# Performance work log

Hardware: AMD Instinct MI355X
Metric: run time of the kernel (lower is better)

The kernel has to match this reference:

```python
import jax, jax.numpy as jnp
import numpy as np
from jax import lax

EPS = 1e-6


def _gaussian_blur(heatmaps, kernel_size):
    # heatmaps: (B, K, H, W). 2D Gaussian conv with 'same' padding, as in the torch code.
    if kernel_size % 2 == 0:
        kernel_size += 1
    B, K, H, W = heatmaps.shape
    sigma = (kernel_size - 1) / 6.0
    coords = jnp.arange(kernel_size, dtype=heatmaps.dtype) - (kernel_size - 1) / 2.0
    g = jnp.exp(-coords ** 2 / (2 * sigma ** 2))
    g = g / g.sum()
    kernel = (g[None, :] * g[:, None])[None, None]  # (1,1,ks,ks)
    pad = kernel_size // 2
    x = heatmaps.reshape(B * K, 1, H, W)
    out = lax.conv_general_dilated(
        x, kernel, window_strides=(1, 1), padding=[(pad, pad), (pad, pad)],
        dimension_numbers=('NCHW', 'OIHW', 'NCHW'))
    return out.reshape(B, K, H, W)


def _dark_forward(heatmaps, kernel_size):
    B, K, H, W = heatmaps.shape
    smooth = _gaussian_blur(heatmaps, kernel_size)
    flat = smooth.reshape(B, K, H * W)
    max_idx = jnp.argmax(flat, axis=-1)            # (B,K) int
    max_vals = jnp.max(flat, axis=-1)              # (B,K)
    y_int = max_idx // W
    x_int = max_idx % W

    # Gather 3x3 patches around the peak (clipped indices; invalid peaks masked below).
    off = jnp.arange(-1, 2)
    yy = jnp.clip(y_int[..., None, None] + off[:, None], 0, H - 1)   # (B,K,3,3)
    xx = jnp.clip(x_int[..., None, None] + off[None, :], 0, W - 1)   # (B,K,3,3)
    lin = (yy * W + xx).reshape(B, K, 9)
    p = jnp.take_along_axis(flat, lin, axis=-1).reshape(B, K, 3, 3)

    dx = (p[..., 1, 2] - p[..., 1, 0]) * 0.5
    dy = (p[..., 2, 1] - p[..., 0, 1]) * 0.5
    dxx = p[..., 1, 2] - 2.0 * p[..., 1, 1] + p[..., 1, 0]
    dyy = p[..., 2, 1] - 2.0 * p[..., 1, 1] + p[..., 0, 1]
    dxy = (p[..., 2, 2] - p[..., 2, 0] - p[..., 0, 2] + p[..., 0, 0]) * 0.25
    det = dxx * dyy - dxy * dxy

    boundary_ok = (x_int >= 1) & (x_int < W - 1) & (y_int >= 1) & (y_int < H - 1)
    valid = boundary_ok & (jnp.abs(det) >= EPS) & (dxx < 0)
    safe_det = jnp.where(valid, det, 1.0)
    off_x = jnp.where(valid, jnp.clip(-(dyy * dx - dxy * dy) / safe_det, -0.5, 0.5), 0.0)
    off_y = jnp.where(valid, jnp.clip(-(dxx * dy - dxy * dx) / safe_det, -0.5, 0.5), 0.0)

    x = jnp.clip(x_int.astype(heatmaps.dtype) + off_x, 0, W - 1)
    y = jnp.clip(y_int.astype(heatmaps.dtype) + off_y, 0, H - 1)
    coords = jnp.stack([x, y], axis=-1)            # (B,K,2)
    return coords, max_vals


def setup_inputs() -> dict:
    key = jax.random.key(0)
    heatmaps = jax.random.normal(key, (64, 17, 256, 192), dtype=jnp.float32)
    return {"heatmaps": heatmaps, "kernel_size": 11}


def reference(heatmaps, kernel_size):
    return _dark_forward(heatmaps, kernel_size)
```

## Files before the change

### kernel.cpp

```cpp
#include <hip/hip_runtime.h>
#include <math.h>

#define H 256
#define W 192
#define BK 1088
#define KS 11
#define NS 4
#define SR 64
#define RING 13

struct GaussW { float g[KS]; };

__device__ __forceinline__ float shflf(float v, int srcLane) {
  return __shfl(v, srcLane & 63, 64);
}

__global__ __launch_bounds__(256) void dark_fused(const float* __restrict__ hm,
                                                  float* __restrict__ out,
                                                  GaussW gw) {
  const int map  = blockIdx.x;
  const int wv   = threadIdx.x >> 6;
  const int lane = threadIdx.x & 63;
  const int y0   = wv * SR;
  const int rs   = y0 - 5;
  const int re   = y0 + SR + 4;
  const float* mbase = hm + (size_t)map * (H * W);
  const float* base  = mbase + 3 * lane;

  float ring[RING][3];

  if (rs >= 0) { const float* p = base + rs * W;
    ring[0][0] = p[0]; ring[0][1] = p[1]; ring[0][2] = p[2];
  } else { ring[0][0] = ring[0][1] = ring[0][2] = 0.f; }
  if (rs + 1 >= 0) { const float* p = base + (rs + 1) * W;
    ring[1][0] = p[0]; ring[1][1] = p[1]; ring[1][2] = p[2];
  } else { ring[1][0] = ring[1][1] = ring[1][2] = 0.f; }

  float bestv = -INFINITY;
  int   besti = 0x7fffffff;

  for (int rb = rs; rb <= re; rb += RING) {
    #pragma unroll
    for (int s = 0; s < RING; ++s) {
      const int rr = rb + s;
      if (rr <= re) {
        {
          const int nr = rr + 2;
          float* slot = ring[(s + 2) % RING];
          if (nr <= re && nr >= 0 && nr < H) {
            const float* p = base + nr * W;
            slot[0] = p[0]; slot[1] = p[1]; slot[2] = p[2];
          } else { slot[0] = slot[1] = slot[2] = 0.f; }
        }
        if (rr >= y0 + 5) {
          float v0 = 0.f, v1 = 0.f, v2 = 0.f;
          #pragma unroll
          for (int i = 0; i < KS; ++i) {
            const float* sl = ring[(s + 3 + i) % RING];
            const float gi = gw.g[i];
            v0 = fmaf(gi, sl[0], v0);
            v1 = fmaf(gi, sl[1], v1);
            v2 = fmaf(gi, sl[2], v2);
          }
          float w13[13];
          w13[5] = v0; w13[6] = v1; w13[7] = v2;
          const float m2b = shflf(v1, lane - 2), m2c = shflf(v2, lane - 2);
          const float m1a = shflf(v0, lane - 1), m1b = shflf(v1, lane - 1), m1c = shflf(v2, lane - 1);
          const float p1a = shflf(v0, lane + 1), p1b = shflf(v1, lane + 1), p1c = shflf(v2, lane + 1);
          const float p2a = shflf(v0, lane + 2), p2b = shflf(v1, lane + 2);
          const bool vm2 = (lane >= 2), vm1 = (lane >= 1);
          const bool vp1 = (lane <= 62), vp2 = (lane <= 61);
          w13[0]  = vm2 ? m2b : 0.f;  w13[1]  = vm2 ? m2c : 0.f;
          w13[2]  = vm1 ? m1a : 0.f;  w13[3]  = vm1 ? m1b : 0.f;  w13[4] = vm1 ? m1c : 0.f;
          w13[8]  = vp1 ? p1a : 0.f;  w13[9]  = vp1 ? p1b : 0.f;  w13[10] = vp1 ? p1c : 0.f;
          w13[11] = vp2 ? p2a : 0.f;  w13[12] = vp2 ? p2b : 0.f;
          const int y = rr - 5;
          #pragma unroll
          for (int c = 0; c < 3; ++c) {
            float hv = 0.f;
            #pragma unroll
            for (int j = 0; j < KS; ++j) hv = fmaf(gw.g[j], w13[c + j], hv);
            const int idx = y * W + 3 * lane + c;
            if (hv > bestv) { bestv = hv; besti = idx; }
          }
        }
      }
    }
  }

  #pragma unroll
  for (int off = 32; off; off >>= 1) {
    const float ov = __shfl_xor(bestv, off, 64);
    const int   oi = __shfl_xor(besti, off, 64);
    if (ov > bestv || (ov == bestv && oi < besti)) { bestv = ov; besti = oi; }
  }

  __shared__ float swv[NS];
  __shared__ int   swi[NS];
  __shared__ float hbuf[39];

  if (lane == 0) { swv[wv] = bestv; swi[wv] = besti; }
  __syncthreads();
  if (wv != 0) return;

  float bv = swv[0]; int bi = swi[0];
  #pragma unroll
  for (int k = 1; k < NS; ++k) {
    const float v = swv[k]; const int ix = swi[k];
    if (v > bv || (v == bv && ix < bi)) { bv = v; bi = ix; }
  }
  const int y = bi / W;
  const int x = bi - y * W;
  const bool interior = (x >= 1) && (x < W - 1) && (y >= 1) && (y < H - 1);

  if (interior) {
    if (lane < 39) {
      const int rl = lane / 3, dxc = lane % 3;
      const int rr = y - 6 + rl;
      const int cc = x - 1 + dxc;
      float hv = 0.f;
      if (rr >= 0 && rr < H) {
        const float* rowp = mbase + rr * W;
        #pragma unroll
        for (int k = 0; k < KS; ++k) {
          const int c2 = cc - 5 + k;
          const float vv = (c2 >= 0 && c2 < W) ? rowp[c2] : 0.f;
          hv = fmaf(gw.g[k], vv, hv);
        }
      }
      hbuf[lane] = hv;
    }
  }

  if (lane == 0) {
    float xf = (float)x, yf = (float)y;
    if (interior) {
      float p[3][3];
      for (int dy = 0; dy < 3; ++dy)
        for (int dx = 0; dx < 3; ++dx) {
          float acc = 0.f;
          #pragma unroll
          for (int i = 0; i < KS; ++i) acc = fmaf(gw.g[i], hbuf[(dy + i) * 3 + dx], acc);
          p[dy][dx] = acc;
        }
      const float d1x = (p[1][2] - p[1][0]) * 0.5f;
      const float d1y = (p[2][1] - p[0][1]) * 0.5f;
      const float dxx = p[1][2] - 2.f * p[1][1] + p[1][0];
      const float dyy = p[2][1] - 2.f * p[1][1] + p[0][1];
      const float dxy = (p[2][2] - p[2][0] - p[0][2] + p[0][0]) * 0.25f;
      const float det = dxx * dyy - dxy * dxy;
      if (fabsf(det) >= 1e-6f && dxx < 0.f) {
        float ox = -(dyy * d1x - dxy * d1y) / det;
        float oy = -(dxx * d1y - dxy * d1x) / det;
        ox = fminf(fmaxf(ox, -0.5f), 0.5f);
        oy = fminf(fmaxf(oy, -0.5f), 0.5f);
        xf += ox; yf += oy;
      }
    }
    xf = fminf(fmaxf(xf, 0.f), (float)(W - 1));
    yf = fminf(fmaxf(yf, 0.f), (float)(H - 1));
    out[2 * map]      = xf;
    out[2 * map + 1]  = yf;
    out[2 * BK + map] = bv;
  }
}

extern "C" void kernel_launch(void* const* d_in, const int* in_sizes, int n_in,
                              void* d_out, int out_size, void* d_ws, size_t ws_size,
                              hipStream_t stream) {
  const float* hm = (const float*)d_in[0];
  float* out = (float*)d_out;
  (void)d_ws; (void)ws_size;

  GaussW gw;
  {
    const double sig = (KS - 1) / 6.0;
    const float denom = (float)(2.0 * sig * sig);
    float g[KS]; float s = 0.f;
    for (int i = 0; i < KS; ++i) {
      const float c = (float)i - (float)((KS - 1) / 2);
      g[i] = expf(-(c * c) / denom);
      s += g[i];
    }
    for (int i = 0; i < KS; ++i) gw.g[i] = g[i] / s;
  }

  dark_fused<<<BK, 256, 0, stream>>>(hm, out, gw);
}
```

Baseline: 308.0 us.

## Scatter vertical blur into rolling accumulators with deeper row prefetch

Replaces the 13-row ring buffer, where each output row re-gathers 11 stored rows, with a scatter formulation. Each loaded row is FMA'd into 11 rotating accumulator rows, and a finished row is emitted once it has received all 11 taps. Row loads are issued 6 iterations ahead instead of 2, so more global-load latency is hidden behind arithmetic. The cost is more live registers (accumulator plus 11-row load buffer), which may lower occupancy or cause spills.

```diff
diff --git a/kernel.cpp b/kernel.cpp
--- a/kernel.cpp
+++ b/kernel.cpp
@@ -7,7 +7,8 @@
 #define KS 11
 #define NS 4
 #define SR 64
-#define RING 13
+#define DP 6
+#define NIT 77
 
 struct GaussW { float g[KS]; };
 
@@ -22,69 +23,87 @@
   const int wv   = threadIdx.x >> 6;
   const int lane = threadIdx.x & 63;
   const int y0   = wv * SR;
-  const int rs   = y0 - 5;
-  const int re   = y0 + SR + 4;
+  const int r0   = y0 - 5;
   const float* mbase = hm + (size_t)map * (H * W);
   const float* base  = mbase + 3 * lane;
-
-  float ring[RING][3];
-
-  if (rs >= 0) { const float* p = base + rs * W;
-    ring[0][0] = p[0]; ring[0][1] = p[1]; ring[0][2] = p[2];
-  } else { ring[0][0] = ring[0][1] = ring[0][2] = 0.f; }
-  if (rs + 1 >= 0) { const float* p = base + (rs + 1) * W;
-    ring[1][0] = p[0]; ring[1][1] = p[1]; ring[1][2] = p[2];
-  } else { ring[1][0] = ring[1][1] = ring[1][2] = 0.f; }
+  const int xb = 3 * lane;
+
+  float acc[11][3];
+  #pragma unroll
+  for (int k = 0; k < 11; ++k) acc[k][0] = acc[k][1] = acc[k][2] = 0.f;
+
+  float lbuf[11][3];
+  #pragma unroll
+  for (int k = 0; k < DP; ++k) {
+    const int r = r0 + k;
+    if (r >= 0 && r < H) {
+      const float* p = base + r * W;
+      lbuf[k][0] = p[0]; lbuf[k][1] = p[1]; lbuf[k][2] = p[2];
+    } else { lbuf[k][0] = lbuf[k][1] = lbuf[k][2] = 0.f; }
+  }
 
   float bestv = -INFINITY;
   int   besti = 0x7fffffff;
 
-  for (int rb = rs; rb <= re; rb += RING) {
+  #pragma unroll 1
+  for (int ob = 0; ob < 7; ++ob) {
     #pragma unroll
-    for (int s = 0; s < RING; ++s) {
-      const int rr = rb + s;
-      if (rr <= re) {
-        {
-          const int nr = rr + 2;
-          float* slot = ring[(s + 2) % RING];
-          if (nr <= re && nr >= 0 && nr < H) {
-            const float* p = base + nr * W;
-            slot[0] = p[0]; slot[1] = p[1]; slot[2] = p[2];
-          } else { slot[0] = slot[1] = slot[2] = 0.f; }
-        }
-        if (rr >= y0 + 5) {
-          float v0 = 0.f, v1 = 0.f, v2 = 0.f;
+    for (int s = 0; s < 11; ++s) {
+      const int t = 11 * ob + s;
+
+      {
+        const int tp = t + DP;
+        if (tp < NIT) {
+          const int r = r0 + tp;
+          if (r >= 0 && r < H) {
+            const float* p = base + r * W;
+            lbuf[(s + DP) % 11][0] = p[0];
+            lbuf[(s + DP) % 11][1] = p[1];
+            lbuf[(s + DP) % 11][2] = p[2];
+          } else {
+            lbuf[(s + DP) % 11][0] = 0.f;
+            lbuf[(s + DP) % 11][1] = 0.f;
+            lbuf[(s + DP) % 11][2] = 0.f;
+          }
+        }
+      }
+
+      {
+        const float a0 = lbuf[s][0], a1 = lbuf[s][1], a2 = lbuf[s][2];
+        #pragma unroll
+        for (int k = 0; k < 11; ++k) {
+          const float gk = gw.g[10 - k];
+          acc[(s + k) % 11][0] = fmaf(gk, a0, acc[(s + k) % 11][0]);
+          acc[(s + k) % 11][1] = fmaf(gk, a1, acc[(s + k) % 11][1]);
+          acc[(s + k) % 11][2] = fmaf(gk, a2, acc[(s + k) % 11][2]);
+        }
+      }
+
+      if (t >= 10 && t <= 73) {
+        const float v0 = acc[s][0], v1 = acc[s][1], v2 = acc[s][2];
+        float w13[13];
+        w13[5] = v0; w13[6] = v1; w13[7] = v2;
+        const float m2b = shflf(v1, lane - 2), m2c = shflf(v2, lane - 2);
+        const float m1a = shflf(v0, lane - 1), m1b = shflf(v1, lane - 1), m1c = shflf(v2, lane - 1);
+        const float p1a = shflf(v0, lane + 1), p1b = shflf(v1, lane + 1), p1c = shflf(v2, lane + 1);
+        const float p2a = shflf(v0, lane + 2), p2b = shflf(v1, lane + 2);
+        const bool vm2 = (lane >= 2), vm1 = (lane >= 1);
+        const bool vp1 = (lane <= 62), vp2 = (lane <= 61);
+        w13[0]  = vm2 ? m2b : 0.f;  w13[1]  = vm2 ? m2c : 0.f;
+        w13[2]  = vm1 ? m1a : 0.f;  w13[3]  = vm1 ? m1b : 0.f;  w13[4] = vm1 ? m1c : 0.f;
+        w13[8]  = vp1 ? p1a : 0.f;  w13[9]  = vp1 ? p1b : 0.f;  w13[10] = vp1 ? p1c : 0.f;
+        w13[11] = vp2 ? p2a : 0.f;  w13[12] = vp2 ? p2b : 0.f;
+        const int y = r0 + t - 5;
+        #pragma unroll
+        for (int c = 0; c < 3; ++c) {
+          float hv = 0.f;
           #pragma unroll
-          for (int i = 0; i < KS; ++i) {
-            const float* sl = ring[(s + 3 + i) % RING];
-            const float gi = gw.g[i];
-            v0 = fmaf(gi, sl[0], v0);
-            v1 = fmaf(gi, sl[1], v1);
-            v2 = fmaf(gi, sl[2], v2);
-          }
-          float w13[13];
-          w13[5] = v0; w13[6] = v1; w13[7] = v2;
-          const float m2b = shflf(v1, lane - 2), m2c = shflf(v2, lane - 2);
-          const float m1a = shflf(v0, lane - 1), m1b = shflf(v1, lane - 1), m1c = shflf(v2, lane - 1);
-          const float p1a = shflf(v0, lane + 1), p1b = shflf(v1, lane + 1), p1c = shflf(v2, lane + 1);
-          const float p2a = shflf(v0, lane + 2), p2b = shflf(v1, lane + 2);
-          const bool vm2 = (lane >= 2), vm1 = (lane >= 1);
-          const bool vp1 = (lane <= 62), vp2 = (lane <= 61);
-          w13[0]  = vm2 ? m2b : 0.f;  w13[1]  = vm2 ? m2c : 0.f;
-          w13[2]  = vm1 ? m1a : 0.f;  w13[3]  = vm1 ? m1b : 0.f;  w13[4] = vm1 ? m1c : 0.f;
-          w13[8]  = vp1 ? p1a : 0.f;  w13[9]  = vp1 ? p1b : 0.f;  w13[10] = vp1 ? p1c : 0.f;
-          w13[11] = vp2 ? p2a : 0.f;  w13[12] = vp2 ? p2b : 0.f;
-          const int y = rr - 5;
-          #pragma unroll
-          for (int c = 0; c < 3; ++c) {
-            float hv = 0.f;
-            #pragma unroll
-            for (int j = 0; j < KS; ++j) hv = fmaf(gw.g[j], w13[c + j], hv);
-            const int idx = y * W + 3 * lane + c;
-            if (hv > bestv) { bestv = hv; besti = idx; }
-          }
-        }
-      }
+          for (int j = 0; j < KS; ++j) hv = fmaf(gw.g[j], w13[c + j], hv);
+          const int idx = y * W + xb + c;
+          if (hv > bestv) { bestv = hv; besti = idx; }
+        }
+      }
+      acc[s][0] = acc[s][1] = acc[s][2] = 0.f;
     }
   }
 
@@ -138,10 +157,10 @@
       float p[3][3];
       for (int dy = 0; dy < 3; ++dy)
         for (int dx = 0; dx < 3; ++dx) {
-          float acc = 0.f;
+          float a = 0.f;
           #pragma unroll
-          for (int i = 0; i < KS; ++i) acc = fmaf(gw.g[i], hbuf[(dy + i) * 3 + dx], acc);
-          p[dy][dx] = acc;
+          for (int i = 0; i < KS; ++i) a = fmaf(gw.g[i], hbuf[(dy + i) * 3 + dx], a);
+          p[dy][dx] = a;
         }
       const float d1x = (p[1][2] - p[1][0]) * 0.5f;
       const float d1y = (p[2][1] - p[0][1]) * 0.5f;
```

After: 328.9 us. +6.8%, slower.

## Split fused kernel into slice-reduction kernel and separate epilogue kernel

Applied to the files above, without the earlier changes.

The single fused kernel, which used 256-thread blocks per map and a block-level reduction, is split into two launches. The first uses 128-thread blocks of two independent slices with a swizzled block-to-slice mapping and writes per-slice maxima to workspace. The second, one wave per map, reduces the four slice results and runs the sub-pixel refinement. The aim is to drop the __syncthreads and the idle-wave tail in the epilogue and to improve occupancy and scheduling, at the cost of an extra launch and a workspace round trip.

```diff
diff --git a/kernel.cpp b/kernel.cpp
--- a/kernel.cpp
+++ b/kernel.cpp
@@ -8,6 +8,8 @@
 #define NS 4
 #define SR 64
 #define RING 13
+#define NSLICE (BK * NS)
+#define NB1 (NSLICE / 2)
 
 struct GaussW { float g[KS]; };
 
@@ -15,11 +17,15 @@
   return __shfl(v, srcLane & 63, 64);
 }
 
-__global__ __launch_bounds__(256) void dark_fused(const float* __restrict__ hm,
-                                                  float* __restrict__ out,
-                                                  GaussW gw) {
-  const int map  = blockIdx.x;
-  const int wv   = threadIdx.x >> 6;
+__global__ __launch_bounds__(128, 4) void dark_slice(const float* __restrict__ hm,
+                                                     float* __restrict__ wsv,
+                                                     int* __restrict__ wsi,
+                                                     GaussW gw) {
+  const int b   = blockIdx.x;
+  const int t2  = (b & 7) * (NB1 / 8) + (b >> 3);
+  const int slc = 2 * t2 + (threadIdx.x >> 6);
+  const int map = slc >> 2;
+  const int wv  = slc & 3;
   const int lane = threadIdx.x & 63;
   const int y0   = wv * SR;
   const int rs   = y0 - 5;
@@ -95,18 +101,24 @@
     if (ov > bestv || (ov == bestv && oi < besti)) { bestv = ov; besti = oi; }
   }
 
-  __shared__ float swv[NS];
-  __shared__ int   swi[NS];
+  if (lane == 0) { wsv[slc] = bestv; wsi[slc] = besti; }
+}
+
+__global__ __launch_bounds__(64) void dark_epi(const float* __restrict__ hm,
+                                               const float* __restrict__ wsv,
+                                               const int* __restrict__ wsi,
+                                               float* __restrict__ out,
+                                               GaussW gw) {
+  const int map  = blockIdx.x;
+  const int lane = threadIdx.x;
+  const float* mbase = hm + (size_t)map * (H * W);
+
   __shared__ float hbuf[39];
 
-  if (lane == 0) { swv[wv] = bestv; swi[wv] = besti; }
-  __syncthreads();
-  if (wv != 0) return;
-
-  float bv = swv[0]; int bi = swi[0];
+  float bv = wsv[4 * map]; int bi = wsi[4 * map];
   #pragma unroll
   for (int k = 1; k < NS; ++k) {
-    const float v = swv[k]; const int ix = swi[k];
+    const float v = wsv[4 * map + k]; const int ix = wsi[4 * map + k];
     if (v > bv || (v == bv && ix < bi)) { bv = v; bi = ix; }
   }
   const int y = bi / W;
@@ -138,10 +150,10 @@
       float p[3][3];
       for (int dy = 0; dy < 3; ++dy)
         for (int dx = 0; dx < 3; ++dx) {
-          float acc = 0.f;
+          float a = 0.f;
           #pragma unroll
-          for (int i = 0; i < KS; ++i) acc = fmaf(gw.g[i], hbuf[(dy + i) * 3 + dx], acc);
-          p[dy][dx] = acc;
+          for (int i = 0; i < KS; ++i) a = fmaf(gw.g[i], hbuf[(dy + i) * 3 + dx], a);
+          p[dy][dx] = a;
         }
       const float d1x = (p[1][2] - p[1][0]) * 0.5f;
       const float d1y = (p[2][1] - p[0][1]) * 0.5f;
@@ -170,7 +182,10 @@
                               hipStream_t stream) {
   const float* hm = (const float*)d_in[0];
   float* out = (float*)d_out;
-  (void)d_ws; (void)ws_size;
+
+  float* wsv = (float*)d_ws;
+  int*   wsi = (int*)((char*)d_ws + NSLICE * sizeof(float));
+  (void)ws_size;
 
   GaussW gw;
   {
@@ -185,5 +200,6 @@
     for (int i = 0; i < KS; ++i) gw.g[i] = g[i] / s;
   }
 
-  dark_fused<<<BK, 256, 0, stream>>>(hm, out, gw);
-}
+  dark_slice<<<NB1, 128, 0, stream>>>(hm, wsv, wsi, gw);
+  dark_epi<<<BK, 64, 0, stream>>>(hm, wsv, wsi, out, gw);
+}
```

After: 313.4 us. No clear change (+1.7%).
